# Optimization experiments

Hardware: AMD Instinct MI355X
Metric: run time of the kernel (lower is better)

## Reference

```python
import jax, jax.numpy as jnp
import numpy as np

B, S, H, E, V, NSTEPS = 8, 128, 512, 512, 32000, 8


def setup_inputs() -> dict:
    key = jax.random.key(0)
    ks = jax.random.split(key, 24)

    def lin(k, fi, fo):
        return (jax.random.normal(k, (fi, fo), jnp.float32) / np.sqrt(fi).astype(np.float32))

    return {
        "input_ids": jax.random.randint(ks[0], (B, S), 0, V),
        "tree_ids": jax.random.randint(ks[1], (B, NSTEPS, 3, S), 0, S),
        "emb": jax.random.normal(ks[2], (V, E), jnp.float32) * 0.02,
        "W_ioux": lin(ks[3], E, 3 * H),
        "W_iouh_r": lin(ks[4], H, 3 * H),
        "b_iouh_r": jnp.zeros((3 * H,), jnp.float32),
        "W_iouh_l": lin(ks[5], H, 3 * H),
        "b_iouh_l": jnp.zeros((3 * H,), jnp.float32),
        "W_fx": lin(ks[6], E, H),
        "W_fh0": lin(ks[7], H, H),
        "b_fh0": jnp.zeros((H,), jnp.float32),
        "W_fh1": lin(ks[8], H, H),
        "b_fh1": jnp.zeros((H,), jnp.float32),
        "W_fh2": lin(ks[9], H, H),
        "b_fh2": jnp.zeros((H,), jnp.float32),
        "W_fh3": lin(ks[10], H, H),
        "b_fh3": jnp.zeros((H,), jnp.float32),
    }


def _scatter_rows(vals, idx):
    # out[b, idx[b, j], k] += vals[b, j, k]  (torch scatter_add_ along dim 1)
    return jax.vmap(lambda v, i: jnp.zeros_like(v).at[i].add(v))(vals, idx)


def _gather_rows(vals, idx):
    # out[b, j, k] = vals[b, idx[b, j], k]  (torch gather along dim 1)
    return jnp.take_along_axis(vals, idx[:, :, None], axis=1)


def _masked_scatter(dest, mask_rows, src):
    # Exact torch masked_scatter_ semantics: flatten mask/src, fill True slots
    # with consecutive elements of flattened src.
    m = jnp.broadcast_to(mask_rows[:, :, None], dest.shape).reshape(-1)
    pos = jnp.clip(jnp.cumsum(m) - 1, 0, None)
    out = jnp.where(m, src.reshape(-1)[pos], dest.reshape(-1))
    return out.reshape(dest.shape)


def reference(input_ids, tree_ids, emb, W_ioux, W_iouh_r, b_iouh_r, W_iouh_l,
              b_iouh_l, W_fx, W_fh0, b_fh0, W_fh1, b_fh1, W_fh2, b_fh2,
              W_fh3, b_fh3):
    x = emb[input_ids]                      # [B, S, E]
    Hs = W_fx.shape[1]
    iou_x = x @ W_ioux                      # [B, S, 3H], loop-invariant
    fx_x = x @ W_fx                         # [B, S, H],  loop-invariant
    h0 = jnp.zeros(x.shape[:2] + (Hs,), x.dtype)
    c0 = jnp.zeros_like(h0)
    steps = jnp.transpose(tree_ids, (1, 0, 2, 3))  # [n_steps, B, 3, S]

    def step(carry, t):
        h, c = carry
        idx_d, idx_r, idx_l = t[:, 0], t[:, 1], t[:, 2]
        iou_hr = h @ W_iouh_r + b_iouh_r
        iou_hl = h @ W_iouh_l + b_iouh_l
        # torch scatter_add_ with an index of width H into a 3H buffer only
        # touches the first H channels -- replicate that exactly.
        scat = _scatter_rows(iou_hr[..., :Hs], idx_r) + _scatter_rows(iou_hl[..., :Hs], idx_l)
        iou = iou_x.at[..., :Hs].add(scat)
        i, o, u = jnp.split(iou, 3, axis=-1)
        i, o, u = jax.nn.sigmoid(i), jax.nn.sigmoid(o), jnp.tanh(u)
        # fh0 and fh1 share idx_r, fh2 and fh3 share idx_l -> fold linearly.
        fh_r = h @ (W_fh0 + W_fh1) + (b_fh0 + b_fh1)
        fh_l = h @ (W_fh2 + W_fh3) + (b_fh2 + b_fh3)
        f = jax.nn.sigmoid(_gather_rows(fx_x, idx_d)
                           + _gather_rows(fh_r, idx_r)
                           + _gather_rows(fh_l, idx_l))
        fc = f * c
        c_full = i * u + _scatter_rows(fc, idx_d)
        h_full = o * jnp.tanh(c_full)
        mask = idx_d != 0
        h_new = _masked_scatter(h, mask, h_full)
        c_new = _masked_scatter(c, mask, c_full)
        return (h_new, c_new), None

    (h, c), _ = jax.lax.scan(step, (h0, c0), steps)
    return h
```

## Files before the change

kernel.cpp:

```cpp
#include <hip/hip_runtime.h>
#include <hip/hip_bf16.h>

#define B_ 8
#define S_ 128
#define H_ 512
#define E_ 512
#define NST 8
#define R_ 1024
#define N2 2048
#define KD 512
#define LDA 72
#define TM 64
#define TN 64

typedef __hip_bfloat16 bf16;
typedef __attribute__((ext_vector_type(8))) short v8s;
typedef __attribute__((ext_vector_type(4))) float v4f;

__device__ __forceinline__ float sigm(float x){ return 1.0f/(1.0f + expf(-x)); }
__device__ __forceinline__ float load_in(const void* p, long long i, int isb){
    return isb ? __bfloat162float(((const bf16*)p)[i]) : ((const float*)p)[i];
}
__device__ __forceinline__ int idx_read(const int* p, int j, int is64){
    return is64 ? p[2*j] : p[j];
}
__device__ __forceinline__ unsigned short f2b(float v){
    bf16 b = __float2bfloat16(v);
    return *(unsigned short*)&b;
}

__global__ void probe_all(const void* t0, const void* t1, const void* t2, const void* t3,
                          const void* t4, const void* t5, const void* t6, const void* t7,
                          const void* t8, const void* t9, const void* t10, const void* t11,
                          const void* t12, const void* t13, const void* t14,
                          const int* __restrict__ ids, const int* __restrict__ tree,
                          int* __restrict__ flags){
    const void* ts[15] = {t0,t1,t2,t3,t4,t5,t6,t7,t8,t9,t10,t11,t12,t13,t14};
    int bid = blockIdx.x, t = threadIdx.x;
    int bad = 0;
    if (bid < 15){
        if (t < 512){
            unsigned short u = ((const unsigned short*)ts[bid])[t];
            bad = (((u >> 7) & 0xFF) >= 140);
        }
    } else {
        const int* p = (bid == 15) ? ids : tree;
        int n = (bid == 15) ? 1024 : 2048;
        for (int j = t; j < n; j += 1024)
            if (j & 1) bad |= (p[j] != 0);
    }
    unsigned long long bl = __ballot(bad);
    __shared__ int acc[16];
    if ((t & 63) == 0) acc[t >> 6] = (bl != 0ull) ? 1 : 0;
    __syncthreads();
    if (t == 0){
        int any = 0;
        for (int w = 0; w < 16; ++w) any |= acc[w];
        flags[(bid < 15) ? bid : (16 + bid - 15)] = (bid < 15) ? (any ? 0 : 1) : (any ? 0 : 1);
    }
}

__global__ void rank_count(const int* __restrict__ tree, int* __restrict__ msk,
                           int* __restrict__ rnk, int* __restrict__ cnt,
                           const int* __restrict__ flags){
    int is64 = flags[17];
    int st = blockIdx.x;
    int t  = threadIdx.x;
    cnt[(0*NST + st)*R_ + t] = 0;
    cnt[(1*NST + st)*R_ + t] = 0;
    cnt[(2*NST + st)*R_ + t] = 0;
    __syncthreads();
    int b = t >> 7, s = t & 127;
    int base = (b*NST + st)*3*S_;
    int d0 = idx_read(tree, base + s, is64);
    int rd = (b<<7) + d0;
    int rr = (b<<7) + idx_read(tree, base + S_ + s, is64);
    int rl = (b<<7) + idx_read(tree, base + 2*S_ + s, is64);
    int m = (d0 != 0) ? 1 : 0;
    unsigned long long bal = __ballot(m);
    int lane = t & 63, wave = t >> 6;
    __shared__ int wtot[16];
    if (lane == 0) wtot[wave] = __popcll(bal);
    __syncthreads();
    int bp = 0;
    for (int w = 0; w < wave; ++w) bp += wtot[w];
    int rank = bp + __popcll(bal & ((1ull << lane) - 1ull));
    msk[st*R_ + t] = m;
    rnk[st*R_ + t] = m ? rank : 0;
    atomicAdd(&cnt[(0*NST + st)*R_ + rr], 1);
    atomicAdd(&cnt[(1*NST + st)*R_ + rl], 1);
    atomicAdd(&cnt[(2*NST + st)*R_ + rd], 1);
}

__global__ void csr_scan(const int* __restrict__ cnt, int* __restrict__ off,
                         int* __restrict__ cur){
    int st = blockIdx.x, a = blockIdx.y;
    int t = threadIdx.x;
    int base = (a*NST + st)*R_;
    __shared__ int sh[R_];
    int v = cnt[base + t];
    sh[t] = v;
    __syncthreads();
    for (int d = 1; d < R_; d <<= 1){
        int x = (t >= d) ? sh[t - d] : 0;
        __syncthreads();
        sh[t] += x;
        __syncthreads();
    }
    int excl = sh[t] - v;
    off[base + t] = excl;
    cur[base + t] = excl;
}

__global__ void csr_fill(const int* __restrict__ tree, int* __restrict__ cur,
                         int* __restrict__ ent, const int* __restrict__ flags){
    int is64 = flags[17];
    int st = blockIdx.x;
    int t = threadIdx.x;
    int b = t >> 7, s = t & 127;
    int base = (b*NST + st)*3*S_;
    int rd = (b<<7) + idx_read(tree, base + s, is64);
    int rr = (b<<7) + idx_read(tree, base + S_ + s, is64);
    int rl = (b<<7) + idx_read(tree, base + 2*S_ + s, is64);
    int p0 = atomicAdd(&cur[(0*NST + st)*R_ + rr], 1);
    ent[(0*NST + st)*R_ + p0] = t;
    int p1 = atomicAdd(&cur[(1*NST + st)*R_ + rl], 1);
    ent[(1*NST + st)*R_ + p1] = t;
    int p2 = atomicAdd(&cur[(2*NST + st)*R_ + rd], 1);
    ent[(2*NST + st)*R_ + p2] = t | (rr << 10) | (rl << 20);
}

__global__ __launch_bounds__(256)
void pack_all(const void* __restrict__ Wioux, const void* __restrict__ Wfx,
              const void* __restrict__ Wr, const void* __restrict__ Wl,
              const void* __restrict__ W0, const void* __restrict__ W1,
              const void* __restrict__ W2, const void* __restrict__ W3,
              const void* __restrict__ br, const void* __restrict__ bl,
              const void* __restrict__ b0, const void* __restrict__ b1,
              const void* __restrict__ b2, const void* __restrict__ b3,
              const int* __restrict__ ids, const void* __restrict__ emb,
              unsigned short* __restrict__ WxT, unsigned short* __restrict__ WcatT,
              float* __restrict__ bcat, unsigned short* __restrict__ xb,
              float* __restrict__ h0, unsigned short* __restrict__ hb,
              const int* __restrict__ flags){
    int bid = blockIdx.x, tid = threadIdx.x;
    if (bid < 512){
        int f_wx = flags[1], f_wf = flags[6];
        int n = (bid & 7)*256 + tid;
        int k0 = (bid >> 3)*8;
        unsigned short tmp[8];
        #pragma unroll
        for (int i = 0; i < 8; ++i){
            float v = (n < 1536) ? load_in(Wioux, (long long)(k0+i)*1536 + n, f_wx)
                                 : load_in(Wfx,   (long long)(k0+i)*512 + (n-1536), f_wf);
            tmp[i] = f2b(v);
        }
        *(v8s*)&WxT[(size_t)n*KD + k0] = *(v8s*)tmp;
    } else if (bid < 1024){
        int fWr=flags[2], fWl=flags[4], fW0=flags[7], fW1=flags[9], fW2=flags[11], fW3=flags[13];
        int bb = bid - 512;
        int n = (bb & 7)*256 + tid;
        int k0 = (bb >> 3)*8;
        unsigned short tmp[8];
        #pragma unroll
        for (int i = 0; i < 8; ++i){
            long long k = k0 + i;
            float v;
            if      (n <  512) v = load_in(Wr, k*1536 + n, fWr);
            else if (n < 1024) v = load_in(Wl, k*1536 + (n-512), fWl);
            else if (n < 1536) { int c = n-1024; v = load_in(W0, k*512+c, fW0) + load_in(W1, k*512+c, fW1); }
            else               { int c = n-1536; v = load_in(W2, k*512+c, fW2) + load_in(W3, k*512+c, fW3); }
            tmp[i] = f2b(v);
        }
        *(v8s*)&WcatT[(size_t)n*KD + k0] = *(v8s*)tmp;
    } else if (bid < 1032){
        int fbr=flags[3], fbl=flags[5], fb0=flags[8], fb1=flags[10], fb2=flags[12], fb3=flags[14];
        int n = (bid - 1024)*256 + tid;
        float v;
        if      (n <  512) v = load_in(br, n, fbr);
        else if (n < 1024) v = load_in(bl, n-512, fbl);
        else if (n < 1536) v = load_in(b0, n-1024, fb0) + load_in(b1, n-1024, fb1);
        else               v = load_in(b2, n-1536, fb2) + load_in(b3, n-1536, fb3);
        bcat[n] = v;
    } else if (bid < 1288){
        int f_emb = flags[0], i64 = flags[16];
        int id = (bid - 1032)*256 + tid;
        int r = id >> 6, c0 = (id & 63)*8;
        long long base = (long long)idx_read(ids, r, i64)*E_ + c0;
        unsigned short tmp[8];
        #pragma unroll
        for (int i = 0; i < 8; ++i) tmp[i] = f2b(load_in(emb, base + i, f_emb));
        *(v8s*)&xb[(size_t)r*KD + c0] = *(v8s*)tmp;
    } else if (bid < 2312){
        int idx = (bid - 1288)*256 + tid;
        ((float4*)h0)[idx] = make_float4(0.f, 0.f, 0.f, 0.f);
    } else {
        int idx = (bid - 2312)*256 + tid;
        ((float4*)hb)[idx] = make_float4(0.f, 0.f, 0.f, 0.f);
    }
}

__global__ __launch_bounds__(256)
void gemm_bf16(const unsigned short* __restrict__ A,
               const unsigned short* __restrict__ BT,
               const float* __restrict__ bias,
               float* __restrict__ C){
    __shared__ short As[TM*LDA];
    __shared__ short Bs[TN*LDA];
    int bn = blockIdx.x, bm = blockIdx.y;
    int tid = threadIdx.x;
    int lane = tid & 63, wave = tid >> 6;
    int wm = wave & 1, wn = wave >> 1;
    int lm = lane & 15, quad = lane >> 4;
    v4f acc[2][2];
    #pragma unroll
    for (int i=0;i<2;++i)
        #pragma unroll
        for (int j=0;j<2;++j) acc[i][j] = (v4f)0.0f;

    int srow = tid >> 3, sg = (tid & 7)*8;
    const unsigned short* Ab = A  + (size_t)(bm*TM)*KD;
    const unsigned short* Bb = BT + (size_t)(bn*TN)*KD;
    v8s pa[2], pb[2];
    #pragma unroll
    for (int j=0;j<2;++j){
        pa[j] = *(const v8s*)(Ab + (size_t)(j*32+srow)*KD + sg);
        pb[j] = *(const v8s*)(Bb + (size_t)(j*32+srow)*KD + sg);
    }
    for (int k0 = 0; k0 < KD; k0 += 64){
        #pragma unroll
        for (int j=0;j<2;++j){
            *(v8s*)&As[(j*32+srow)*LDA + sg] = pa[j];
            *(v8s*)&Bs[(j*32+srow)*LDA + sg] = pb[j];
        }
        __syncthreads();
        int k1 = k0 + 64;
        if (k1 < KD){
            #pragma unroll
            for (int j=0;j<2;++j){
                pa[j] = *(const v8s*)(Ab + (size_t)(j*32+srow)*KD + k1 + sg);
                pb[j] = *(const v8s*)(Bb + (size_t)(j*32+srow)*KD + k1 + sg);
            }
        }
        #pragma unroll
        for (int kk = 0; kk < 64; kk += 32){
            v8s af[2], bf[2];
            #pragma unroll
            for (int i=0;i<2;++i){
                af[i] = *(const v8s*)&As[(wm*32 + i*16 + lm)*LDA + kk + quad*8];
                bf[i] = *(const v8s*)&Bs[(wn*32 + i*16 + lm)*LDA + kk + quad*8];
            }
            #pragma unroll
            for (int i=0;i<2;++i)
                #pragma unroll
                for (int j=0;j<2;++j)
                    acc[i][j] = __builtin_amdgcn_mfma_f32_16x16x32_bf16(af[i], bf[j], acc[i][j], 0, 0, 0);
        }
        __syncthreads();
    }
    #pragma unroll
    for (int j=0;j<2;++j){
        int n = bn*TN + wn*32 + j*16 + lm;
        float bv = bias ? bias[n] : 0.0f;
        #pragma unroll
        for (int i=0;i<2;++i){
            int m0 = bm*TM + wm*32 + i*16 + quad*4;
            #pragma unroll
            for (int rg = 0; rg < 4; ++rg)
                C[(size_t)(m0+rg)*N2 + n] = acc[i][j][rg] + bv;
        }
    }
}

__global__ __launch_bounds__(256)
void step_fused(const float* __restrict__ XO, const float* __restrict__ T,
                const float* __restrict__ h_old, const float* __restrict__ c_old,
                float* __restrict__ h_new, float* __restrict__ c_new,
                unsigned short* __restrict__ hb,
                const int* __restrict__ msk, const int* __restrict__ rnk,
                const int* __restrict__ cnt, const int* __restrict__ off,
                const int* __restrict__ ent, int st){
    int r = blockIdx.x;
    if (!msk[st*R_ + r]){
        for (int c = threadIdx.x; c < H_; c += 256){
            float hv = h_old[(size_t)r*H_ + c];
            h_new[(size_t)r*H_ + c] = hv;
            c_new[(size_t)r*H_ + c] = c_old[(size_t)r*H_ + c];
            hb[(size_t)r*KD + c] = f2b(hv);
        }
        return;
    }
    int j = rnk[st*R_ + r];
    int bR = off[(0*NST + st)*R_ + j], dR = cnt[(0*NST + st)*R_ + j];
    int bL = off[(1*NST + st)*R_ + j], dL = cnt[(1*NST + st)*R_ + j];
    int bD = off[(2*NST + st)*R_ + j], dD = cnt[(2*NST + st)*R_ + j];
    const int* eR = ent + (0*NST + st)*R_ + bR;
    const int* eL = ent + (1*NST + st)*R_ + bL;
    const int* eD = ent + (2*NST + st)*R_ + bD;
    const float* xo = XO + (size_t)j*N2;
    for (int c = threadIdx.x; c < H_; c += 256){
        float scat = 0.f;
        for (int e = 0; e < dR; ++e) scat += T[(size_t)eR[e]*N2 + c];
        for (int e = 0; e < dL; ++e) scat += T[(size_t)eL[e]*N2 + 512 + c];
        float fxv = xo[1536 + c];
        float csc = 0.f;
        for (int e = 0; e < dD; ++e){
            int pk = eD[e];
            int s  = pk & 1023, rr = (pk >> 10) & 1023, rl = (pk >> 20) & 1023;
            float f = sigm(fxv + T[(size_t)rr*N2 + 1024 + c] + T[(size_t)rl*N2 + 1536 + c]);
            csc += f * c_old[(size_t)s*H_ + c];
        }
        float ig = sigm(xo[c] + scat);
        float og = sigm(xo[512 + c]);
        float ug = tanhf(xo[1024 + c]);
        float cf = ig*ug + csc;
        float hf = og * tanhf(cf);
        h_new[(size_t)r*H_ + c] = hf;
        c_new[(size_t)r*H_ + c] = cf;
        hb[(size_t)r*KD + c] = f2b(hf);
    }
}

extern "C" void kernel_launch(void* const* d_in, const int* in_sizes, int n_in,
                              void* d_out, int out_size, void* d_ws, size_t ws_size,
                              hipStream_t stream) {
    const int* input_ids = (const int*)d_in[0];
    const int* tree      = (const int*)d_in[1];

    char* p = (char*)d_ws;
    auto alloc = [&](size_t bytes) -> void* {
        void* q = (void*)p;
        p += (bytes + 255) & ~(size_t)255;
        return q;
    };
    float*          XO     = (float*)alloc((size_t)R_*N2*4);
    float*          T      = (float*)alloc((size_t)R_*N2*4);
    float*          h0     = (float*)alloc((size_t)R_*H_*4);
    float*          c0     = (float*)alloc((size_t)R_*H_*4);
    float*          h1     = (float*)alloc((size_t)R_*H_*4);
    float*          c1     = (float*)alloc((size_t)R_*H_*4);
    unsigned short* WxT    = (unsigned short*)alloc((size_t)N2*KD*2);
    unsigned short* WcatT  = (unsigned short*)alloc((size_t)N2*KD*2);
    float*          bcat   = (float*)alloc((size_t)N2*4);
    unsigned short* xb     = (unsigned short*)alloc((size_t)R_*KD*2);
    unsigned short* hb     = (unsigned short*)alloc((size_t)R_*KD*2);
    int*            msk    = (int*)alloc((size_t)NST*R_*4);
    int*            rnk    = (int*)alloc((size_t)NST*R_*4);
    int*            cnt    = (int*)alloc((size_t)3*NST*R_*4);
    int*            off    = (int*)alloc((size_t)3*NST*R_*4);
    int*            cur    = (int*)alloc((size_t)3*NST*R_*4);
    int*            ent    = (int*)alloc((size_t)3*NST*R_*4);
    int*            flags  = (int*)alloc(256);

    hipLaunchKernelGGL(probe_all, dim3(17), dim3(1024), 0, stream,
                       d_in[2], d_in[3], d_in[4], d_in[5], d_in[6], d_in[7], d_in[8],
                       d_in[9], d_in[10], d_in[11], d_in[12], d_in[13], d_in[14],
                       d_in[15], d_in[16], input_ids, tree, flags);
    hipLaunchKernelGGL(rank_count, dim3(NST), dim3(R_), 0, stream, tree, msk, rnk, cnt, flags);
    hipLaunchKernelGGL(csr_scan, dim3(NST, 3), dim3(R_), 0, stream, cnt, off, cur);
    hipLaunchKernelGGL(csr_fill, dim3(NST), dim3(R_), 0, stream, tree, cur, ent, flags);
    hipLaunchKernelGGL(pack_all, dim3(2568), dim3(256), 0, stream,
                       d_in[3], d_in[8],
                       d_in[4], d_in[6], d_in[9], d_in[11], d_in[13], d_in[15],
                       d_in[5], d_in[7], d_in[10], d_in[12], d_in[14], d_in[16],
                       input_ids, d_in[2],
                       WxT, WcatT, bcat, xb, h0, hb, flags);

    hipLaunchKernelGGL(gemm_bf16, dim3(N2/TN, R_/TM), dim3(256), 0, stream,
                       xb, WxT, (const float*)nullptr, XO);

    float *hc = h0, *cc = c0, *hn = h1, *cn = c1;
    for (int st = 0; st < NST; ++st){
        hipLaunchKernelGGL(gemm_bf16, dim3(N2/TN, R_/TM), dim3(256), 0, stream,
                           hb, WcatT, bcat, T);
        hipLaunchKernelGGL(step_fused, dim3(R_), dim3(256), 0, stream,
                           XO, T, hc, cc, hn, cn, hb, msk, rnk, cnt, off, ent, st);
        float* th = hc; hc = hn; hn = th;
        float* tc = cc; cc = cn; cn = tc;
    }
    hipMemcpyAsync(d_out, hc, (size_t)R_*H_*4, hipMemcpyDeviceToDevice, stream);
}
```

Measured before the change: 324.8 us.

## Fuse all stages into one persistent cooperative kernel with grid syncs

The separate probe, CSR-build, pack, GEMM and per-step launches are merged into a single cooperative kernel of 256 blocks. Stages are separated by grid-wide syncs instead of kernel boundaries, and the final device-to-device copy is folded into the last step's writes. The GEMM tile becomes 64x128 with 512 threads so the 256 resident blocks cover the output exactly. This targets launch and inter-kernel gap overhead across roughly twenty launches, at the cost of grid-sync latency and less parallelism in the per-step elementwise phase, which now uses 4 rows per block.

```diff
diff --git a/kernel.cpp b/kernel.cpp
--- a/kernel.cpp
+++ b/kernel.cpp
@@ -1,5 +1,8 @@
 #include <hip/hip_runtime.h>
 #include <hip/hip_bf16.h>
+#include <hip/hip_cooperative_groups.h>
+
+namespace cg = cooperative_groups;
 
 #define B_ 8
 #define S_ 128
@@ -10,13 +13,26 @@
 #define N2 2048
 #define KD 512
 #define LDA 72
-#define TM 64
-#define TN 64
+#define NBLK 256
+#define NTHR 512
+#define GS (NBLK*NTHR)
 
 typedef __hip_bfloat16 bf16;
 typedef __attribute__((ext_vector_type(8))) short v8s;
 typedef __attribute__((ext_vector_type(4))) float v4f;
 
+struct Params {
+  const int* ids; const int* tree;
+  const void* emb; const void* Wioux; const void* Wr; const void* br;
+  const void* Wl;  const void* bl;    const void* Wfx;
+  const void* W0;  const void* b0;    const void* W1; const void* b1;
+  const void* W2;  const void* b2;    const void* W3; const void* b3;
+  float* XO; float* T; float* h0; float* c0; float* h1; float* c1; float* bcat;
+  unsigned short* WxT; unsigned short* WcatT; unsigned short* xb; unsigned short* hb;
+  int* msk; int* rnk; int* cnt; int* off; int* cur; int* ent; int* flags;
+  float* out;
+};
+
 __device__ __forceinline__ float sigm(float x){ return 1.0f/(1.0f + expf(-x)); }
 __device__ __forceinline__ float load_in(const void* p, long long i, int isb){
     return isb ? __bfloat162float(((const bf16*)p)[i]) : ((const float*)p)[i];
@@ -29,186 +45,12 @@
     return *(unsigned short*)&b;
 }
 
-__global__ void probe_all(const void* t0, const void* t1, const void* t2, const void* t3,
-                          const void* t4, const void* t5, const void* t6, const void* t7,
-                          const void* t8, const void* t9, const void* t10, const void* t11,
-                          const void* t12, const void* t13, const void* t14,
-                          const int* __restrict__ ids, const int* __restrict__ tree,
-                          int* __restrict__ flags){
-    const void* ts[15] = {t0,t1,t2,t3,t4,t5,t6,t7,t8,t9,t10,t11,t12,t13,t14};
-    int bid = blockIdx.x, t = threadIdx.x;
-    int bad = 0;
-    if (bid < 15){
-        if (t < 512){
-            unsigned short u = ((const unsigned short*)ts[bid])[t];
-            bad = (((u >> 7) & 0xFF) >= 140);
-        }
-    } else {
-        const int* p = (bid == 15) ? ids : tree;
-        int n = (bid == 15) ? 1024 : 2048;
-        for (int j = t; j < n; j += 1024)
-            if (j & 1) bad |= (p[j] != 0);
-    }
-    unsigned long long bl = __ballot(bad);
-    __shared__ int acc[16];
-    if ((t & 63) == 0) acc[t >> 6] = (bl != 0ull) ? 1 : 0;
-    __syncthreads();
-    if (t == 0){
-        int any = 0;
-        for (int w = 0; w < 16; ++w) any |= acc[w];
-        flags[(bid < 15) ? bid : (16 + bid - 15)] = (bid < 15) ? (any ? 0 : 1) : (any ? 0 : 1);
-    }
-}
-
-__global__ void rank_count(const int* __restrict__ tree, int* __restrict__ msk,
-                           int* __restrict__ rnk, int* __restrict__ cnt,
-                           const int* __restrict__ flags){
-    int is64 = flags[17];
-    int st = blockIdx.x;
-    int t  = threadIdx.x;
-    cnt[(0*NST + st)*R_ + t] = 0;
-    cnt[(1*NST + st)*R_ + t] = 0;
-    cnt[(2*NST + st)*R_ + t] = 0;
-    __syncthreads();
-    int b = t >> 7, s = t & 127;
-    int base = (b*NST + st)*3*S_;
-    int d0 = idx_read(tree, base + s, is64);
-    int rd = (b<<7) + d0;
-    int rr = (b<<7) + idx_read(tree, base + S_ + s, is64);
-    int rl = (b<<7) + idx_read(tree, base + 2*S_ + s, is64);
-    int m = (d0 != 0) ? 1 : 0;
-    unsigned long long bal = __ballot(m);
-    int lane = t & 63, wave = t >> 6;
-    __shared__ int wtot[16];
-    if (lane == 0) wtot[wave] = __popcll(bal);
-    __syncthreads();
-    int bp = 0;
-    for (int w = 0; w < wave; ++w) bp += wtot[w];
-    int rank = bp + __popcll(bal & ((1ull << lane) - 1ull));
-    msk[st*R_ + t] = m;
-    rnk[st*R_ + t] = m ? rank : 0;
-    atomicAdd(&cnt[(0*NST + st)*R_ + rr], 1);
-    atomicAdd(&cnt[(1*NST + st)*R_ + rl], 1);
-    atomicAdd(&cnt[(2*NST + st)*R_ + rd], 1);
-}
-
-__global__ void csr_scan(const int* __restrict__ cnt, int* __restrict__ off,
-                         int* __restrict__ cur){
-    int st = blockIdx.x, a = blockIdx.y;
-    int t = threadIdx.x;
-    int base = (a*NST + st)*R_;
-    __shared__ int sh[R_];
-    int v = cnt[base + t];
-    sh[t] = v;
-    __syncthreads();
-    for (int d = 1; d < R_; d <<= 1){
-        int x = (t >= d) ? sh[t - d] : 0;
-        __syncthreads();
-        sh[t] += x;
-        __syncthreads();
-    }
-    int excl = sh[t] - v;
-    off[base + t] = excl;
-    cur[base + t] = excl;
-}
-
-__global__ void csr_fill(const int* __restrict__ tree, int* __restrict__ cur,
-                         int* __restrict__ ent, const int* __restrict__ flags){
-    int is64 = flags[17];
-    int st = blockIdx.x;
-    int t = threadIdx.x;
-    int b = t >> 7, s = t & 127;
-    int base = (b*NST + st)*3*S_;
-    int rd = (b<<7) + idx_read(tree, base + s, is64);
-    int rr = (b<<7) + idx_read(tree, base + S_ + s, is64);
-    int rl = (b<<7) + idx_read(tree, base + 2*S_ + s, is64);
-    int p0 = atomicAdd(&cur[(0*NST + st)*R_ + rr], 1);
-    ent[(0*NST + st)*R_ + p0] = t;
-    int p1 = atomicAdd(&cur[(1*NST + st)*R_ + rl], 1);
-    ent[(1*NST + st)*R_ + p1] = t;
-    int p2 = atomicAdd(&cur[(2*NST + st)*R_ + rd], 1);
-    ent[(2*NST + st)*R_ + p2] = t | (rr << 10) | (rl << 20);
-}
-
-__global__ __launch_bounds__(256)
-void pack_all(const void* __restrict__ Wioux, const void* __restrict__ Wfx,
-              const void* __restrict__ Wr, const void* __restrict__ Wl,
-              const void* __restrict__ W0, const void* __restrict__ W1,
-              const void* __restrict__ W2, const void* __restrict__ W3,
-              const void* __restrict__ br, const void* __restrict__ bl,
-              const void* __restrict__ b0, const void* __restrict__ b1,
-              const void* __restrict__ b2, const void* __restrict__ b3,
-              const int* __restrict__ ids, const void* __restrict__ emb,
-              unsigned short* __restrict__ WxT, unsigned short* __restrict__ WcatT,
-              float* __restrict__ bcat, unsigned short* __restrict__ xb,
-              float* __restrict__ h0, unsigned short* __restrict__ hb,
-              const int* __restrict__ flags){
-    int bid = blockIdx.x, tid = threadIdx.x;
-    if (bid < 512){
-        int f_wx = flags[1], f_wf = flags[6];
-        int n = (bid & 7)*256 + tid;
-        int k0 = (bid >> 3)*8;
-        unsigned short tmp[8];
-        #pragma unroll
-        for (int i = 0; i < 8; ++i){
-            float v = (n < 1536) ? load_in(Wioux, (long long)(k0+i)*1536 + n, f_wx)
-                                 : load_in(Wfx,   (long long)(k0+i)*512 + (n-1536), f_wf);
-            tmp[i] = f2b(v);
-        }
-        *(v8s*)&WxT[(size_t)n*KD + k0] = *(v8s*)tmp;
-    } else if (bid < 1024){
-        int fWr=flags[2], fWl=flags[4], fW0=flags[7], fW1=flags[9], fW2=flags[11], fW3=flags[13];
-        int bb = bid - 512;
-        int n = (bb & 7)*256 + tid;
-        int k0 = (bb >> 3)*8;
-        unsigned short tmp[8];
-        #pragma unroll
-        for (int i = 0; i < 8; ++i){
-            long long k = k0 + i;
-            float v;
-            if      (n <  512) v = load_in(Wr, k*1536 + n, fWr);
-            else if (n < 1024) v = load_in(Wl, k*1536 + (n-512), fWl);
-            else if (n < 1536) { int c = n-1024; v = load_in(W0, k*512+c, fW0) + load_in(W1, k*512+c, fW1); }
-            else               { int c = n-1536; v = load_in(W2, k*512+c, fW2) + load_in(W3, k*512+c, fW3); }
-            tmp[i] = f2b(v);
-        }
-        *(v8s*)&WcatT[(size_t)n*KD + k0] = *(v8s*)tmp;
-    } else if (bid < 1032){
-        int fbr=flags[3], fbl=flags[5], fb0=flags[8], fb1=flags[10], fb2=flags[12], fb3=flags[14];
-        int n = (bid - 1024)*256 + tid;
-        float v;
-        if      (n <  512) v = load_in(br, n, fbr);
-        else if (n < 1024) v = load_in(bl, n-512, fbl);
-        else if (n < 1536) v = load_in(b0, n-1024, fb0) + load_in(b1, n-1024, fb1);
-        else               v = load_in(b2, n-1536, fb2) + load_in(b3, n-1536, fb3);
-        bcat[n] = v;
-    } else if (bid < 1288){
-        int f_emb = flags[0], i64 = flags[16];
-        int id = (bid - 1032)*256 + tid;
-        int r = id >> 6, c0 = (id & 63)*8;
-        long long base = (long long)idx_read(ids, r, i64)*E_ + c0;
-        unsigned short tmp[8];
-        #pragma unroll
-        for (int i = 0; i < 8; ++i) tmp[i] = f2b(load_in(emb, base + i, f_emb));
-        *(v8s*)&xb[(size_t)r*KD + c0] = *(v8s*)tmp;
-    } else if (bid < 2312){
-        int idx = (bid - 1288)*256 + tid;
-        ((float4*)h0)[idx] = make_float4(0.f, 0.f, 0.f, 0.f);
-    } else {
-        int idx = (bid - 2312)*256 + tid;
-        ((float4*)hb)[idx] = make_float4(0.f, 0.f, 0.f, 0.f);
-    }
-}
-
-__global__ __launch_bounds__(256)
-void gemm_bf16(const unsigned short* __restrict__ A,
-               const unsigned short* __restrict__ BT,
-               const float* __restrict__ bias,
-               float* __restrict__ C){
-    __shared__ short As[TM*LDA];
-    __shared__ short Bs[TN*LDA];
-    int bn = blockIdx.x, bm = blockIdx.y;
-    int tid = threadIdx.x;
+__device__ __forceinline__ void gemm_tile(const unsigned short* __restrict__ A,
+                                          const unsigned short* __restrict__ BT,
+                                          const float* __restrict__ bias,
+                                          float* __restrict__ C,
+                                          int bid, int tid, short* As, short* Bs){
+    int bm = bid >> 4, bn = bid & 15;
     int lane = tid & 63, wave = tid >> 6;
     int wm = wave & 1, wn = wave >> 1;
     int lm = lane & 15, quad = lane >> 4;
@@ -219,28 +61,23 @@
         for (int j=0;j<2;++j) acc[i][j] = (v4f)0.0f;
 
     int srow = tid >> 3, sg = (tid & 7)*8;
-    const unsigned short* Ab = A  + (size_t)(bm*TM)*KD;
-    const unsigned short* Bb = BT + (size_t)(bn*TN)*KD;
-    v8s pa[2], pb[2];
-    #pragma unroll
-    for (int j=0;j<2;++j){
-        pa[j] = *(const v8s*)(Ab + (size_t)(j*32+srow)*KD + sg);
-        pb[j] = *(const v8s*)(Bb + (size_t)(j*32+srow)*KD + sg);
-    }
+    const unsigned short* Ab = A  + (size_t)(bm*64)*KD;
+    const unsigned short* Bb = BT + (size_t)(bn*128)*KD;
+    v8s pa, pb0, pb1;
+    pa  = *(const v8s*)(Ab + (size_t)srow*KD + sg);
+    pb0 = *(const v8s*)(Bb + (size_t)srow*KD + sg);
+    pb1 = *(const v8s*)(Bb + (size_t)(64+srow)*KD + sg);
     for (int k0 = 0; k0 < KD; k0 += 64){
-        #pragma unroll
-        for (int j=0;j<2;++j){
-            *(v8s*)&As[(j*32+srow)*LDA + sg] = pa[j];
-            *(v8s*)&Bs[(j*32+srow)*LDA + sg] = pb[j];
-        }
+        __syncthreads();
+        *(v8s*)&As[srow*LDA + sg] = pa;
+        *(v8s*)&Bs[srow*LDA + sg] = pb0;
+        *(v8s*)&Bs[(64+srow)*LDA + sg] = pb1;
         __syncthreads();
         int k1 = k0 + 64;
         if (k1 < KD){
-            #pragma unroll
-            for (int j=0;j<2;++j){
-                pa[j] = *(const v8s*)(Ab + (size_t)(j*32+srow)*KD + k1 + sg);
-                pb[j] = *(const v8s*)(Bb + (size_t)(j*32+srow)*KD + k1 + sg);
-            }
+            pa  = *(const v8s*)(Ab + (size_t)srow*KD + k1 + sg);
+            pb0 = *(const v8s*)(Bb + (size_t)srow*KD + k1 + sg);
+            pb1 = *(const v8s*)(Bb + (size_t)(64+srow)*KD + k1 + sg);
         }
         #pragma unroll
         for (int kk = 0; kk < 64; kk += 32){
@@ -256,15 +93,14 @@
                 for (int j=0;j<2;++j)
                     acc[i][j] = __builtin_amdgcn_mfma_f32_16x16x32_bf16(af[i], bf[j], acc[i][j], 0, 0, 0);
         }
-        __syncthreads();
     }
     #pragma unroll
     for (int j=0;j<2;++j){
-        int n = bn*TN + wn*32 + j*16 + lm;
+        int n = bn*128 + wn*32 + j*16 + lm;
         float bv = bias ? bias[n] : 0.0f;
         #pragma unroll
         for (int i=0;i<2;++i){
-            int m0 = bm*TM + wm*32 + i*16 + quad*4;
+            int m0 = bm*64 + wm*32 + i*16 + quad*4;
             #pragma unroll
             for (int rg = 0; rg < 4; ++rg)
                 C[(size_t)(m0+rg)*N2 + n] = acc[i][j][rg] + bv;
@@ -272,65 +108,230 @@
     }
 }
 
-__global__ __launch_bounds__(256)
-void step_fused(const float* __restrict__ XO, const float* __restrict__ T,
-                const float* __restrict__ h_old, const float* __restrict__ c_old,
-                float* __restrict__ h_new, float* __restrict__ c_new,
-                unsigned short* __restrict__ hb,
-                const int* __restrict__ msk, const int* __restrict__ rnk,
-                const int* __restrict__ cnt, const int* __restrict__ off,
-                const int* __restrict__ ent, int st){
-    int r = blockIdx.x;
-    if (!msk[st*R_ + r]){
-        for (int c = threadIdx.x; c < H_; c += 256){
-            float hv = h_old[(size_t)r*H_ + c];
-            h_new[(size_t)r*H_ + c] = hv;
-            c_new[(size_t)r*H_ + c] = c_old[(size_t)r*H_ + c];
-            hb[(size_t)r*KD + c] = f2b(hv);
-        }
-        return;
-    }
-    int j = rnk[st*R_ + r];
-    int bR = off[(0*NST + st)*R_ + j], dR = cnt[(0*NST + st)*R_ + j];
-    int bL = off[(1*NST + st)*R_ + j], dL = cnt[(1*NST + st)*R_ + j];
-    int bD = off[(2*NST + st)*R_ + j], dD = cnt[(2*NST + st)*R_ + j];
-    const int* eR = ent + (0*NST + st)*R_ + bR;
-    const int* eL = ent + (1*NST + st)*R_ + bL;
-    const int* eD = ent + (2*NST + st)*R_ + bD;
-    const float* xo = XO + (size_t)j*N2;
-    for (int c = threadIdx.x; c < H_; c += 256){
-        float scat = 0.f;
-        for (int e = 0; e < dR; ++e) scat += T[(size_t)eR[e]*N2 + c];
-        for (int e = 0; e < dL; ++e) scat += T[(size_t)eL[e]*N2 + 512 + c];
-        float fxv = xo[1536 + c];
-        float csc = 0.f;
-        for (int e = 0; e < dD; ++e){
-            int pk = eD[e];
-            int s  = pk & 1023, rr = (pk >> 10) & 1023, rl = (pk >> 20) & 1023;
-            float f = sigm(fxv + T[(size_t)rr*N2 + 1024 + c] + T[(size_t)rl*N2 + 1536 + c]);
-            csc += f * c_old[(size_t)s*H_ + c];
-        }
-        float ig = sigm(xo[c] + scat);
-        float og = sigm(xo[512 + c]);
-        float ug = tanhf(xo[1024 + c]);
-        float cf = ig*ug + csc;
-        float hf = og * tanhf(cf);
-        h_new[(size_t)r*H_ + c] = hf;
-        c_new[(size_t)r*H_ + c] = cf;
-        hb[(size_t)r*KD + c] = f2b(hf);
+__global__ __launch_bounds__(NTHR, 2) void mega(Params p){
+    cg::grid_group gg = cg::this_grid();
+    int bid = blockIdx.x, tid = threadIdx.x;
+    __shared__ short As[64*LDA];
+    __shared__ short Bs[128*LDA];
+    __shared__ int aux[NTHR];
+    __shared__ int wt[8];
+
+    if (bid < 17){
+        const void* ts[15] = {p.emb,p.Wioux,p.Wr,p.br,p.Wl,p.bl,p.Wfx,
+                              p.W0,p.b0,p.W1,p.b1,p.W2,p.b2,p.W3,p.b3};
+        int bad = 0;
+        if (bid < 15){
+            unsigned short u = ((const unsigned short*)ts[bid])[tid];
+            bad = (((u >> 7) & 0xFF) >= 140);
+        } else {
+            const int* q = (bid == 15) ? p.ids : p.tree;
+            int n = (bid == 15) ? 1024 : 2048;
+            for (int j = tid; j < n; j += NTHR) if (j & 1) bad |= (q[j] != 0);
+        }
+        unsigned long long bl_ = __ballot(bad);
+        if ((tid & 63) == 0) wt[tid >> 6] = (bl_ != 0ull) ? 1 : 0;
+        __syncthreads();
+        if (tid == 0){
+            int any = 0;
+            for (int w = 0; w < 8; ++w) any |= wt[w];
+            p.flags[(bid < 15) ? bid : (16 + bid - 15)] = any ? 0 : 1;
+        }
+    }
+    gg.sync();
+
+    int is64 = p.flags[17];
+
+    if (bid < 8){
+        int st = bid;
+        for (int c = tid; c < R_; c += NTHR){
+            p.cnt[(0*NST + st)*R_ + c] = 0;
+            p.cnt[(1*NST + st)*R_ + c] = 0;
+            p.cnt[(2*NST + st)*R_ + c] = 0;
+        }
+        __syncthreads();
+        int runbase = 0;
+        for (int ch = 0; ch < 2; ++ch){
+            int t = ch*NTHR + tid;
+            int b = t >> 7, s = t & 127;
+            int base = (b*NST + st)*3*S_;
+            int d0 = idx_read(p.tree, base + s, is64);
+            int rd = (b<<7) + d0;
+            int rr = (b<<7) + idx_read(p.tree, base + S_ + s, is64);
+            int rl = (b<<7) + idx_read(p.tree, base + 2*S_ + s, is64);
+            int m = (d0 != 0) ? 1 : 0;
+            unsigned long long bal = __ballot(m);
+            int lane = tid & 63, wv = tid >> 6;
+            if (lane == 0) wt[wv] = __popcll(bal);
+            __syncthreads();
+            int bp = runbase, tot = 0;
+            for (int w = 0; w < wv; ++w) bp += wt[w];
+            for (int w = 0; w < 8; ++w) tot += wt[w];
+            int rank = bp + __popcll(bal & ((1ull << lane) - 1ull));
+            p.msk[st*R_ + t] = m;
+            p.rnk[st*R_ + t] = m ? rank : 0;
+            atomicAdd(&p.cnt[(0*NST + st)*R_ + rr], 1);
+            atomicAdd(&p.cnt[(1*NST + st)*R_ + rl], 1);
+            atomicAdd(&p.cnt[(2*NST + st)*R_ + rd], 1);
+            runbase += tot;
+            __syncthreads();
+        }
+    }
+    {
+        int gt = bid*NTHR + tid;
+        int f_wx = p.flags[1], f_wf = p.flags[6];
+        for (int u = gt; u < 131072; u += GS){
+            int n = u >> 6, k0 = (u & 63)*8;
+            unsigned short tmp[8];
+            #pragma unroll
+            for (int i = 0; i < 8; ++i){
+                float v = (n < 1536) ? load_in(p.Wioux, (long long)(k0+i)*1536 + n, f_wx)
+                                     : load_in(p.Wfx,   (long long)(k0+i)*512 + (n-1536), f_wf);
+                tmp[i] = f2b(v);
+            }
+            *(v8s*)&p.WxT[(size_t)n*KD + k0] = *(v8s*)tmp;
+        }
+        int fWr=p.flags[2], fWl=p.flags[4], fW0=p.flags[7], fW1=p.flags[9], fW2=p.flags[11], fW3=p.flags[13];
+        for (int u = gt; u < 131072; u += GS){
+            int n = u >> 6, k0 = (u & 63)*8;
+            unsigned short tmp[8];
+            #pragma unroll
+            for (int i = 0; i < 8; ++i){
+                long long k = k0 + i;
+                float v;
+                if      (n <  512) v = load_in(p.Wr, k*1536 + n, fWr);
+                else if (n < 1024) v = load_in(p.Wl, k*1536 + (n-512), fWl);
+                else if (n < 1536) { int c = n-1024; v = load_in(p.W0, k*512+c, fW0) + load_in(p.W1, k*512+c, fW1); }
+                else               { int c = n-1536; v = load_in(p.W2, k*512+c, fW2) + load_in(p.W3, k*512+c, fW3); }
+                tmp[i] = f2b(v);
+            }
+            *(v8s*)&p.WcatT[(size_t)n*KD + k0] = *(v8s*)tmp;
+        }
+        int fbr=p.flags[3], fbl=p.flags[5], fb0=p.flags[8], fb1=p.flags[10], fb2=p.flags[12], fb3=p.flags[14];
+        for (int n = gt; n < 2048; n += GS){
+            float v;
+            if      (n <  512) v = load_in(p.br, n, fbr);
+            else if (n < 1024) v = load_in(p.bl, n-512, fbl);
+            else if (n < 1536) v = load_in(p.b0, n-1024, fb0) + load_in(p.b1, n-1024, fb1);
+            else               v = load_in(p.b2, n-1536, fb2) + load_in(p.b3, n-1536, fb3);
+            p.bcat[n] = v;
+        }
+        int f_emb = p.flags[0], i64i = p.flags[16];
+        for (int u = gt; u < 65536; u += GS){
+            int r = u >> 6, c0 = (u & 63)*8;
+            long long base = (long long)idx_read(p.ids, r, i64i)*E_ + c0;
+            unsigned short tmp[8];
+            #pragma unroll
+            for (int i = 0; i < 8; ++i) tmp[i] = f2b(load_in(p.emb, base + i, f_emb));
+            *(v8s*)&p.xb[(size_t)r*KD + c0] = *(v8s*)tmp;
+        }
+        for (int u = gt; u < 262144; u += GS)
+            ((float4*)p.h0)[u] = make_float4(0.f,0.f,0.f,0.f);
+        for (int u = gt; u < 65536; u += GS)
+            ((float4*)p.hb)[u] = make_float4(0.f,0.f,0.f,0.f);
+    }
+    gg.sync();
+
+    if (bid < 24){
+        int a = bid >> 3, st = bid & 7;
+        int base = (a*NST + st)*R_;
+        int v0 = p.cnt[base + tid*2], v1 = p.cnt[base + tid*2 + 1];
+        int tot = v0 + v1;
+        aux[tid] = tot;
+        __syncthreads();
+        for (int d = 1; d < NTHR; d <<= 1){
+            int x = (tid >= d) ? aux[tid - d] : 0;
+            __syncthreads();
+            aux[tid] += x;
+            __syncthreads();
+        }
+        int excl = aux[tid] - tot;
+        p.off[base + tid*2]     = excl;      p.cur[base + tid*2]     = excl;
+        p.off[base + tid*2 + 1] = excl + v0; p.cur[base + tid*2 + 1] = excl + v0;
+    }
+    gemm_tile(p.xb, p.WxT, (const float*)0, p.XO, bid, tid, As, Bs);
+    gg.sync();
+
+    if (bid < 8){
+        int st = bid;
+        for (int ch = 0; ch < 2; ++ch){
+            int t = ch*NTHR + tid;
+            int b = t >> 7, s = t & 127;
+            int base = (b*NST + st)*3*S_;
+            int rd = (b<<7) + idx_read(p.tree, base + s, is64);
+            int rr = (b<<7) + idx_read(p.tree, base + S_ + s, is64);
+            int rl = (b<<7) + idx_read(p.tree, base + 2*S_ + s, is64);
+            int p0 = atomicAdd(&p.cur[(0*NST + st)*R_ + rr], 1);
+            p.ent[(0*NST + st)*R_ + p0] = t;
+            int p1 = atomicAdd(&p.cur[(1*NST + st)*R_ + rl], 1);
+            p.ent[(1*NST + st)*R_ + p1] = t;
+            int p2 = atomicAdd(&p.cur[(2*NST + st)*R_ + rd], 1);
+            p.ent[(2*NST + st)*R_ + p2] = t | (rr << 10) | (rl << 20);
+        }
+    }
+    gemm_tile(p.hb, p.WcatT, p.bcat, p.T, bid, tid, As, Bs);
+    gg.sync();
+
+    float *hc = p.h0, *cc = p.c0, *hn = p.h1, *cn = p.c1;
+    for (int st = 0; st < NST; ++st){
+        for (int q = 0; q < 4; ++q){
+            int r = bid*4 + q;
+            int c = tid;
+            if (!p.msk[st*R_ + r]){
+                float hv = hc[(size_t)r*H_ + c];
+                float cv = cc[(size_t)r*H_ + c];
+                hn[(size_t)r*H_ + c] = hv;
+                cn[(size_t)r*H_ + c] = cv;
+                p.hb[(size_t)r*KD + c] = f2b(hv);
+                if (st == NST-1) p.out[(size_t)r*H_ + c] = hv;
+            } else {
+                int j = p.rnk[st*R_ + r];
+                int bR = p.off[(0*NST+st)*R_ + j], dR = p.cnt[(0*NST+st)*R_ + j];
+                int bL = p.off[(1*NST+st)*R_ + j], dL = p.cnt[(1*NST+st)*R_ + j];
+                int bD = p.off[(2*NST+st)*R_ + j], dD = p.cnt[(2*NST+st)*R_ + j];
+                const int* eR = p.ent + (0*NST+st)*R_ + bR;
+                const int* eL = p.ent + (1*NST+st)*R_ + bL;
+                const int* eD = p.ent + (2*NST+st)*R_ + bD;
+                const float* xo = p.XO + (size_t)j*N2;
+                float scv = 0.f;
+                for (int e = 0; e < dR; ++e) scv += p.T[(size_t)eR[e]*N2 + c];
+                for (int e = 0; e < dL; ++e) scv += p.T[(size_t)eL[e]*N2 + 512 + c];
+                float fxv = xo[1536 + c];
+                float csc = 0.f;
+                for (int e = 0; e < dD; ++e){
+                    int pk = eD[e];
+                    int s  = pk & 1023, rr = (pk >> 10) & 1023, rl = (pk >> 20) & 1023;
+                    float f = sigm(fxv + p.T[(size_t)rr*N2 + 1024 + c]
+                                       + p.T[(size_t)rl*N2 + 1536 + c]);
+                    csc += f * cc[(size_t)s*H_ + c];
+                }
+                float ig = sigm(xo[c] + scv);
+                float og = sigm(xo[512 + c]);
+                float ug = tanhf(xo[1024 + c]);
+                float cf = ig*ug + csc;
+                float hf = og * tanhf(cf);
+                hn[(size_t)r*H_ + c] = hf;
+                cn[(size_t)r*H_ + c] = cf;
+                p.hb[(size_t)r*KD + c] = f2b(hf);
+                if (st == NST-1) p.out[(size_t)r*H_ + c] = hf;
+            }
+        }
+        gg.sync();
+        if (st < NST-1){
+            gemm_tile(p.hb, p.WcatT, p.bcat, p.T, bid, tid, As, Bs);
+            gg.sync();
+        }
+        float* t1 = hc; hc = hn; hn = t1;
+        float* t2 = cc; cc = cn; cn = t2;
     }
 }
 
 extern "C" void kernel_launch(void* const* d_in, const int* in_sizes, int n_in,
                               void* d_out, int out_size, void* d_ws, size_t ws_size,
                               hipStream_t stream) {
-    const int* input_ids = (const int*)d_in[0];
-    const int* tree      = (const int*)d_in[1];
-
-    char* p = (char*)d_ws;
+    char* wp = (char*)d_ws;
     auto alloc = [&](size_t bytes) -> void* {
-        void* q = (void*)p;
-        p += (bytes + 255) & ~(size_t)255;
+        void* q = (void*)wp;
+        wp += (bytes + 255) & ~(size_t)255;
         return q;
     };
     float*          XO     = (float*)alloc((size_t)R_*N2*4);
@@ -352,31 +353,23 @@
     int*            ent    = (int*)alloc((size_t)3*NST*R_*4);
     int*            flags  = (int*)alloc(256);
 
-    hipLaunchKernelGGL(probe_all, dim3(17), dim3(1024), 0, stream,
-                       d_in[2], d_in[3], d_in[4], d_in[5], d_in[6], d_in[7], d_in[8],
-                       d_in[9], d_in[10], d_in[11], d_in[12], d_in[13], d_in[14],
-                       d_in[15], d_in[16], input_ids, tree, flags);
-    hipLaunchKernelGGL(rank_count, dim3(NST), dim3(R_), 0, stream, tree, msk, rnk, cnt, flags);
-    hipLaunchKernelGGL(csr_scan, dim3(NST, 3), dim3(R_), 0, stream, cnt, off, cur);
-    hipLaunchKernelGGL(csr_fill, dim3(NST), dim3(R_), 0, stream, tree, cur, ent, flags);
-    hipLaunchKernelGGL(pack_all, dim3(2568), dim3(256), 0, stream,
-                       d_in[3], d_in[8],
-                       d_in[4], d_in[6], d_in[9], d_in[11], d_in[13], d_in[15],
-                       d_in[5], d_in[7], d_in[10], d_in[12], d_in[14], d_in[16],
-                       input_ids, d_in[2],
-                       WxT, WcatT, bcat, xb, h0, hb, flags);
-
-    hipLaunchKernelGGL(gemm_bf16, dim3(N2/TN, R_/TM), dim3(256), 0, stream,
-                       xb, WxT, (const float*)nullptr, XO);
-
-    float *hc = h0, *cc = c0, *hn = h1, *cn = c1;
-    for (int st = 0; st < NST; ++st){
-        hipLaunchKernelGGL(gemm_bf16, dim3(N2/TN, R_/TM), dim3(256), 0, stream,
-                           hb, WcatT, bcat, T);
-        hipLaunchKernelGGL(step_fused, dim3(R_), dim3(256), 0, stream,
-                           XO, T, hc, cc, hn, cn, hb, msk, rnk, cnt, off, ent, st);
-        float* th = hc; hc = hn; hn = th;
-        float* tc = cc; cc = cn; cn = tc;
-    }
-    hipMemcpyAsync(d_out, hc, (size_t)R_*H_*4, hipMemcpyDeviceToDevice, stream);
-}
+    Params prm;
+    prm.ids = (const int*)d_in[0];  prm.tree = (const int*)d_in[1];
+    prm.emb = d_in[2];  prm.Wioux = d_in[3];
+    prm.Wr  = d_in[4];  prm.br = d_in[5];
+    prm.Wl  = d_in[6];  prm.bl = d_in[7];
+    prm.Wfx = d_in[8];
+    prm.W0 = d_in[9];   prm.b0 = d_in[10];
+    prm.W1 = d_in[11];  prm.b1 = d_in[12];
+    prm.W2 = d_in[13];  prm.b2 = d_in[14];
+    prm.W3 = d_in[15];  prm.b3 = d_in[16];
+    prm.XO = XO; prm.T = T; prm.h0 = h0; prm.c0 = c0; prm.h1 = h1; prm.c1 = c1;
+    prm.bcat = bcat; prm.WxT = WxT; prm.WcatT = WcatT; prm.xb = xb; prm.hb = hb;
+    prm.msk = msk; prm.rnk = rnk; prm.cnt = cnt; prm.off = off; prm.cur = cur;
+    prm.ent = ent; prm.flags = flags;
+    prm.out = (float*)d_out;
+
+    void* kargs[] = { (void*)&prm };
+    hipLaunchCooperativeKernel((const void*)mega, dim3(NBLK), dim3(NTHR),
+                               kargs, 0, stream);
+}
```

New measurement: 928.1 us. 2.86x slower.
